# Performance work log

Measured on AMD Instinct MI355X. Metric: run time of the kernel, lower is better.

## Reference

```python
import jax, jax.numpy as jnp
import numpy as np

IN_CH = 4096
OUT_CH = 4096
DENSITY = 0.1
BATCH = 8192


def setup_inputs() -> dict:
    key = jax.random.key(0)
    k_mask, k_w, k_b, k_x = jax.random.split(key, 4)
    # Fixed sparsity pattern, as in the torch module's sparse_mask.nonzero()
    mask = jax.random.bernoulli(k_mask, DENSITY, (OUT_CH, IN_CH))
    rows, cols = jnp.nonzero(mask)  # unique (row, col) pairs
    rows = rows.astype(jnp.int32)
    cols = cols.astype(jnp.int32)
    nnz = rows.shape[0]
    # Kaiming-style init per output row (approximate: uniform bound from mean fan-in)
    fan_in = jnp.maximum(jnp.sum(mask, axis=1).astype(jnp.float32), 1.0)  # [OUT_CH]
    gain = np.sqrt(2.0 / (1.0 + 5.0))  # leaky_relu gain with a=sqrt(5)
    std = gain / jnp.sqrt(fan_in)
    w_bound = np.sqrt(3.0) * std  # per-row bound
    u = jax.random.uniform(k_w, (nnz,), minval=-1.0, maxval=1.0)
    sparse_weight = u * w_bound[rows]
    b_bound = 1.0 / jnp.sqrt(fan_in)
    bias = jax.random.uniform(k_b, (OUT_CH,), minval=-1.0, maxval=1.0) * b_bound
    x = jax.random.normal(k_x, (BATCH, IN_CH), dtype=jnp.float32)
    return {
        "x": x,
        "sparse_weight": sparse_weight.astype(jnp.float32),
        "rows": rows,
        "cols": cols,
        "bias": bias.astype(jnp.float32),
    }


def reference(x, sparse_weight, rows, cols, bias):
    # Rebuild the (fixed-pattern) sparse weight as a dense [OUT_CH, IN_CH] matrix
    # (indices are unique, so .set matches the COO semantics), then y = x @ W^T + b.
    W = jnp.zeros((OUT_CH, IN_CH), dtype=sparse_weight.dtype).at[rows, cols].set(sparse_weight)
    return x @ W.T + bias  # [BATCH, OUT_CH]
```

## Files before the change

### kernel.cpp

```cpp
#include <hip/hip_runtime.h>
#include <hip/hip_bf16.h>

#define M_DIM 8192
#define N_DIM 4096
#define K_DIM 4096
#define BM 128
#define BN 128
#define BK 32

typedef __bf16 bf16x8 __attribute__((ext_vector_type(8)));
typedef float  f32x4  __attribute__((ext_vector_type(4)));
typedef unsigned short u16x8 __attribute__((ext_vector_type(8)));

#define ASYNC16(g, l)                                                          \
  __builtin_amdgcn_global_load_lds(                                            \
      (__attribute__((address_space(1))) void*)(g),                            \
      (__attribute__((address_space(3))) void*)(l), 16, 0, 0)

static __device__ __forceinline__ unsigned short f2bf(float f) {
  unsigned int u = __float_as_uint(f);
  u += 0x7fffu + ((u >> 16) & 1u);
  return (unsigned short)(u >> 16);
}

__global__ __launch_bounds__(256) void sl_prep(
    const float4* __restrict__ x4, u16x8* __restrict__ xb,
    const float* __restrict__ vals, const int* __restrict__ rows,
    const int* __restrict__ cols, unsigned short* __restrict__ W, int nnz) {
  const int b = blockIdx.x;
  if (b < N_DIM) {
    __shared__ __align__(16) unsigned short rowbuf[K_DIM];
    u16x8* rb8 = (u16x8*)rowbuf;
    u16x8 z = {};
    rb8[threadIdx.x] = z;
    rb8[256 + threadIdx.x] = z;
    __syncthreads();
    int l = 0, h = nnz;
    while (l < h) { int m = (l + h) >> 1; if (rows[m] < b) l = m + 1; else h = m; }
    const int s = l;
    h = nnz;
    while (l < h) { int m = (l + h) >> 1; if (rows[m] <= b) l = m + 1; else h = m; }
    const int e = l;
    for (int k = s + threadIdx.x; k < e; k += 256)
      rowbuf[cols[k]] = f2bf(vals[k]);
    __syncthreads();
    u16x8* dst = (u16x8*)(W + (size_t)b * K_DIM);
    dst[threadIdx.x] = rb8[threadIdx.x];
    dst[256 + threadIdx.x] = rb8[256 + threadIdx.x];
  } else {
    const int i = (b - N_DIM) * 256 + threadIdx.x;
    float4 a = x4[2 * i];
    float4 c = x4[2 * i + 1];
    u16x8 o;
    o[0] = f2bf(a.x); o[1] = f2bf(a.y); o[2] = f2bf(a.z); o[3] = f2bf(a.w);
    o[4] = f2bf(c.x); o[5] = f2bf(c.y); o[6] = f2bf(c.z); o[7] = f2bf(c.w);
    xb[i] = o;
  }
}

__global__ __launch_bounds__(256) void sl_gemm_bias(
    const unsigned short* __restrict__ A,
    const unsigned short* __restrict__ B,
    const float* __restrict__ bias,
    float* __restrict__ C) {
  __shared__ __align__(16) unsigned short As[BM * BK];
  __shared__ __align__(16) unsigned short Bs[BN * BK];

  const int tid  = threadIdx.x;
  const int wave = tid >> 6;
  const int lane = tid & 63;
  const int m0 = blockIdx.x * BM;
  const int n0 = blockIdx.y * BN;

  const int srow = tid >> 2;
  const int scol = ((tid & 3) ^ ((tid >> 3) & 3)) * 8;
  const unsigned short* gA0 = A + (size_t)(m0 + srow) * K_DIM + scol;
  const unsigned short* gA1 = gA0 + (size_t)64 * K_DIM;
  const unsigned short* gB0 = B + (size_t)(n0 + srow) * K_DIM + scol;
  const unsigned short* gB1 = gB0 + (size_t)64 * K_DIM;
  unsigned short* lA0 = As + (size_t)(wave * 64) * 8;
  unsigned short* lA1 = As + (size_t)(256 + wave * 64) * 8;
  unsigned short* lB0 = Bs + (size_t)(wave * 64) * 8;
  unsigned short* lB1 = Bs + (size_t)(256 + wave * 64) * 8;

  const int wm   = (wave >> 1) * 64;
  const int wn   = (wave & 1) * 64;
  const int fm   = lane & 15;
  const int quad = lane >> 4;
  const int sw   = (fm >> 1) & 3;
  const int kc   = (quad ^ sw) * 8;

  f32x4 acc[4][4] = {};

  for (int k0 = 0; k0 < K_DIM; k0 += BK) {
    ASYNC16(gA0, lA0);
    ASYNC16(gA1, lA1);
    ASYNC16(gB0, lB0);
    ASYNC16(gB1, lB1);
    gA0 += BK; gA1 += BK; gB0 += BK; gB1 += BK;
    __syncthreads();

    bf16x8 af[4], bfr[4];
#pragma unroll
    for (int t = 0; t < 4; ++t) {
      af[t]  = *(const bf16x8*)(As + (size_t)(wm + t * 16 + fm) * BK + kc);
      bfr[t] = *(const bf16x8*)(Bs + (size_t)(wn + t * 16 + fm) * BK + kc);
    }
#pragma unroll
    for (int tm = 0; tm < 4; ++tm)
#pragma unroll
      for (int tn = 0; tn < 4; ++tn)
        acc[tm][tn] = __builtin_amdgcn_mfma_f32_16x16x32_bf16(
            af[tm], bfr[tn], acc[tm][tn], 0, 0, 0);
    __syncthreads();
  }

  float bv[4];
#pragma unroll
  for (int tn = 0; tn < 4; ++tn) bv[tn] = bias[n0 + wn + tn * 16 + fm];

#pragma unroll
  for (int tm = 0; tm < 4; ++tm) {
    const int mbase = m0 + wm + tm * 16 + quad * 4;
#pragma unroll
    for (int tn = 0; tn < 4; ++tn) {
      const int n = n0 + wn + tn * 16 + fm;
      float* p = C + (size_t)mbase * N_DIM + n;
#pragma unroll
      for (int r = 0; r < 4; ++r)
        p[(size_t)r * N_DIM] = acc[tm][tn][r] + bv[tn];
    }
  }
}

__global__ void sl_naive(const float* __restrict__ x, const float* __restrict__ vals,
                         const int* __restrict__ rows, const int* __restrict__ cols,
                         const float* __restrict__ bias, float* __restrict__ out,
                         int nnz) {
  const int o = blockIdx.x;
  int l = 0, h = nnz;
  while (l < h) { int m = (l + h) >> 1; if (rows[m] < o) l = m + 1; else h = m; }
  const int s = l;
  h = nnz;
  while (l < h) { int m = (l + h) >> 1; if (rows[m] <= o) l = m + 1; else h = m; }
  const int e = l;
  const float bv = bias[o];
  for (int b = threadIdx.x; b < M_DIM; b += blockDim.x) {
    float acc = bv;
    const float* xb = x + (size_t)b * K_DIM;
    for (int k = s; k < e; ++k) acc += vals[k] * xb[cols[k]];
    out[(size_t)b * N_DIM + o] = acc;
  }
}

extern "C" void kernel_launch(void* const* d_in, const int* in_sizes, int n_in,
                              void* d_out, int out_size, void* d_ws, size_t ws_size,
                              hipStream_t stream) {
  const float* x    = (const float*)d_in[0];
  const float* vals = (const float*)d_in[1];
  const int*   rows = (const int*)d_in[2];
  const int*   cols = (const int*)d_in[3];
  const float* bias = (const float*)d_in[4];
  float* out = (float*)d_out;
  const int nnz = in_sizes[1];

  const size_t xb_bytes = (size_t)M_DIM * K_DIM * 2;
  const size_t w_bytes  = (size_t)N_DIM * K_DIM * 2;

  if (ws_size >= xb_bytes + w_bytes) {
    unsigned short* xb = (unsigned short*)d_ws;
    unsigned short* W  = (unsigned short*)((char*)d_ws + xb_bytes);

    const int cvt_blocks = (M_DIM * K_DIM) / 8 / 256;
    sl_prep<<<N_DIM + cvt_blocks, 256, 0, stream>>>(
        (const float4*)x, (u16x8*)xb, vals, rows, cols, W, nnz);
    sl_gemm_bias<<<dim3(M_DIM / BM, N_DIM / BN), 256, 0, stream>>>(xb, W, bias, out);
  } else {
    sl_naive<<<N_DIM, 256, 0, stream>>>(x, vals, rows, cols, bias, out, nnz);
  }
}
```

Before: 561.4 us.

## Double-buffer GEMM K loop with BK=64, precompute row bounds, nontemporal stores

The GEMM tile depth goes from 32 to 64 with a wider XOR swizzle. The loop now issues the next tile's async global-to-LDS loads right after fragments are read into registers, so memory traffic overlaps the MFMA work, and occupancy is hinted at 3 blocks. Row start and end offsets are computed once by a small kernel instead of a binary search per block, and output stores use nontemporal hints. This adds a memset and an extra launch, and raises register and LDS pressure.

```diff
diff --git a/kernel.cpp b/kernel.cpp
--- a/kernel.cpp
+++ b/kernel.cpp
@@ -6,7 +6,7 @@
 #define K_DIM 4096
 #define BM 128
 #define BN 128
-#define BK 32
+#define BK 64
 
 typedef __bf16 bf16x8 __attribute__((ext_vector_type(8)));
 typedef float  f32x4  __attribute__((ext_vector_type(4)));
@@ -23,10 +23,20 @@
   return (unsigned short)(u >> 16);
 }
 
+__global__ void sl_bounds(const int* __restrict__ rows, int* __restrict__ row_start,
+                          int* __restrict__ row_end, int nnz) {
+  int k = blockIdx.x * 256 + threadIdx.x;
+  if (k >= nnz) return;
+  int r = rows[k];
+  if (k == 0 || rows[k - 1] != r) row_start[r] = k;
+  if (k == nnz - 1 || rows[k + 1] != r) row_end[r] = k + 1;
+}
+
 __global__ __launch_bounds__(256) void sl_prep(
     const float4* __restrict__ x4, u16x8* __restrict__ xb,
-    const float* __restrict__ vals, const int* __restrict__ rows,
-    const int* __restrict__ cols, unsigned short* __restrict__ W, int nnz) {
+    const float* __restrict__ vals, const int* __restrict__ cols,
+    const int* __restrict__ row_start, const int* __restrict__ row_end,
+    unsigned short* __restrict__ W) {
   const int b = blockIdx.x;
   if (b < N_DIM) {
     __shared__ __align__(16) unsigned short rowbuf[K_DIM];
@@ -35,12 +45,8 @@
     rb8[threadIdx.x] = z;
     rb8[256 + threadIdx.x] = z;
     __syncthreads();
-    int l = 0, h = nnz;
-    while (l < h) { int m = (l + h) >> 1; if (rows[m] < b) l = m + 1; else h = m; }
-    const int s = l;
-    h = nnz;
-    while (l < h) { int m = (l + h) >> 1; if (rows[m] <= b) l = m + 1; else h = m; }
-    const int e = l;
+    const int s = row_start[b];
+    const int e = row_end[b];
     for (int k = s + threadIdx.x; k < e; k += 256)
       rowbuf[cols[k]] = f2bf(vals[k]);
     __syncthreads();
@@ -58,7 +64,42 @@
   }
 }
 
-__global__ __launch_bounds__(256) void sl_gemm_bias(
+__global__ __launch_bounds__(256) void sl_prep_bs(
+    const float4* __restrict__ x4, u16x8* __restrict__ xb,
+    const float* __restrict__ vals, const int* __restrict__ rows,
+    const int* __restrict__ cols, unsigned short* __restrict__ W, int nnz) {
+  const int b = blockIdx.x;
+  if (b < N_DIM) {
+    __shared__ __align__(16) unsigned short rowbuf[K_DIM];
+    u16x8* rb8 = (u16x8*)rowbuf;
+    u16x8 z = {};
+    rb8[threadIdx.x] = z;
+    rb8[256 + threadIdx.x] = z;
+    __syncthreads();
+    int l = 0, h = nnz;
+    while (l < h) { int m = (l + h) >> 1; if (rows[m] < b) l = m + 1; else h = m; }
+    const int s = l;
+    h = nnz;
+    while (l < h) { int m = (l + h) >> 1; if (rows[m] <= b) l = m + 1; else h = m; }
+    const int e = l;
+    for (int k = s + threadIdx.x; k < e; k += 256)
+      rowbuf[cols[k]] = f2bf(vals[k]);
+    __syncthreads();
+    u16x8* dst = (u16x8*)(W + (size_t)b * K_DIM);
+    dst[threadIdx.x] = rb8[threadIdx.x];
+    dst[256 + threadIdx.x] = rb8[256 + threadIdx.x];
+  } else {
+    const int i = (b - N_DIM) * 256 + threadIdx.x;
+    float4 a = x4[2 * i];
+    float4 c = x4[2 * i + 1];
+    u16x8 o;
+    o[0] = f2bf(a.x); o[1] = f2bf(a.y); o[2] = f2bf(a.z); o[3] = f2bf(a.w);
+    o[4] = f2bf(c.x); o[5] = f2bf(c.y); o[6] = f2bf(c.z); o[7] = f2bf(c.w);
+    xb[i] = o;
+  }
+}
+
+__global__ __launch_bounds__(256, 3) void sl_gemm_bias(
     const unsigned short* __restrict__ A,
     const unsigned short* __restrict__ B,
     const float* __restrict__ bias,
@@ -72,47 +113,62 @@
   const int m0 = blockIdx.x * BM;
   const int n0 = blockIdx.y * BN;
 
-  const int srow = tid >> 2;
-  const int scol = ((tid & 3) ^ ((tid >> 3) & 3)) * 8;
-  const unsigned short* gA0 = A + (size_t)(m0 + srow) * K_DIM + scol;
-  const unsigned short* gA1 = gA0 + (size_t)64 * K_DIM;
-  const unsigned short* gB0 = B + (size_t)(n0 + srow) * K_DIM + scol;
-  const unsigned short* gB1 = gB0 + (size_t)64 * K_DIM;
-  unsigned short* lA0 = As + (size_t)(wave * 64) * 8;
-  unsigned short* lA1 = As + (size_t)(256 + wave * 64) * 8;
-  unsigned short* lB0 = Bs + (size_t)(wave * 64) * 8;
-  unsigned short* lB1 = Bs + (size_t)(256 + wave * 64) * 8;
+  const int srow = tid >> 3;
+  const int scol = ((tid & 7) ^ ((tid >> 3) & 7)) * 8;
+  const unsigned short* gA = A + (size_t)(m0 + srow) * K_DIM + scol;
+  const unsigned short* gB = B + (size_t)(n0 + srow) * K_DIM + scol;
+  unsigned short* lA = As + (size_t)(wave * 64) * 8;
+  unsigned short* lB = Bs + (size_t)(wave * 64) * 8;
+  const size_t GROW = (size_t)32 * K_DIM;
+  const size_t LROW = (size_t)256 * 8;
 
   const int wm   = (wave >> 1) * 64;
   const int wn   = (wave & 1) * 64;
   const int fm   = lane & 15;
   const int quad = lane >> 4;
-  const int sw   = (fm >> 1) & 3;
-  const int kc   = (quad ^ sw) * 8;
+  const int sw   = fm & 7;
 
   f32x4 acc[4][4] = {};
 
+#pragma unroll
+  for (int r = 0; r < 4; ++r) {
+    ASYNC16(gA + r * GROW, lA + r * LROW);
+    ASYNC16(gB + r * GROW, lB + r * LROW);
+  }
+  gA += BK; gB += BK;
+
   for (int k0 = 0; k0 < K_DIM; k0 += BK) {
-    ASYNC16(gA0, lA0);
-    ASYNC16(gA1, lA1);
-    ASYNC16(gB0, lB0);
-    ASYNC16(gB1, lB1);
-    gA0 += BK; gA1 += BK; gB0 += BK; gB1 += BK;
-    __syncthreads();
-
-    bf16x8 af[4], bfr[4];
+    __syncthreads();
+
+    bf16x8 af[4][2], bfr[4][2];
 #pragma unroll
     for (int t = 0; t < 4; ++t) {
-      af[t]  = *(const bf16x8*)(As + (size_t)(wm + t * 16 + fm) * BK + kc);
-      bfr[t] = *(const bf16x8*)(Bs + (size_t)(wn + t * 16 + fm) * BK + kc);
+#pragma unroll
+      for (int h = 0; h < 2; ++h) {
+        const int pA = ((h * 4 + quad) ^ sw) * 8;
+        af[t][h]  = *(const bf16x8*)(As + (size_t)(wm + t * 16 + fm) * BK + pA);
+        bfr[t][h] = *(const bf16x8*)(Bs + (size_t)(wn + t * 16 + fm) * BK + pA);
+      }
     }
-#pragma unroll
-    for (int tm = 0; tm < 4; ++tm)
-#pragma unroll
-      for (int tn = 0; tn < 4; ++tn)
-        acc[tm][tn] = __builtin_amdgcn_mfma_f32_16x16x32_bf16(
-            af[tm], bfr[tn], acc[tm][tn], 0, 0, 0);
-    __syncthreads();
+    __syncthreads();
+
+    if (k0 + BK < K_DIM) {
+#pragma unroll
+      for (int r = 0; r < 4; ++r) {
+        ASYNC16(gA + r * GROW, lA + r * LROW);
+        ASYNC16(gB + r * GROW, lB + r * LROW);
+      }
+      gA += BK; gB += BK;
+    }
+
+#pragma unroll
+    for (int h = 0; h < 2; ++h)
+#pragma unroll
+      for (int tm = 0; tm < 4; ++tm)
+#pragma unroll
+        for (int tn = 0; tn < 4; ++tn)
+          acc[tm][tn] = __builtin_amdgcn_mfma_f32_16x16x32_bf16(
+              af[tm][h], bfr[tn][h], acc[tm][tn], 0, 0, 0);
   }
 
   float bv[4];
@@ -128,7 +184,7 @@
       float* p = C + (size_t)mbase * N_DIM + n;
 #pragma unroll
       for (int r = 0; r < 4; ++r)
-        p[(size_t)r * N_DIM] = acc[tm][tn][r] + bv[tn];
+        __builtin_nontemporal_store(acc[tm][tn][r] + bv[tn], p + (size_t)r * N_DIM);
     }
   }
 }
@@ -164,15 +220,27 @@
   float* out = (float*)d_out;
   const int nnz = in_sizes[1];
 
-  const size_t xb_bytes = (size_t)M_DIM * K_DIM * 2;
-  const size_t w_bytes  = (size_t)N_DIM * K_DIM * 2;
-
-  if (ws_size >= xb_bytes + w_bytes) {
+  const size_t xb_bytes  = (size_t)M_DIM * K_DIM * 2;
+  const size_t w_bytes   = (size_t)N_DIM * K_DIM * 2;
+  const size_t idx_bytes = (size_t)2 * N_DIM * 4;
+
+  const int cvt_blocks = (M_DIM * K_DIM) / 8 / 256;
+
+  if (ws_size >= xb_bytes + w_bytes + idx_bytes) {
     unsigned short* xb = (unsigned short*)d_ws;
     unsigned short* W  = (unsigned short*)((char*)d_ws + xb_bytes);
-
-    const int cvt_blocks = (M_DIM * K_DIM) / 8 / 256;
+    int* row_start = (int*)((char*)d_ws + xb_bytes + w_bytes);
+    int* row_end   = row_start + N_DIM;
+
+    hipMemsetAsync(row_start, 0, idx_bytes, stream);
+    sl_bounds<<<(nnz + 255) / 256, 256, 0, stream>>>(rows, row_start, row_end, nnz);
     sl_prep<<<N_DIM + cvt_blocks, 256, 0, stream>>>(
+        (const float4*)x, (u16x8*)xb, vals, cols, row_start, row_end, W);
+    sl_gemm_bias<<<dim3(M_DIM / BM, N_DIM / BN), 256, 0, stream>>>(xb, W, bias, out);
+  } else if (ws_size >= xb_bytes + w_bytes) {
+    unsigned short* xb = (unsigned short*)d_ws;
+    unsigned short* W  = (unsigned short*)((char*)d_ws + xb_bytes);
+    sl_prep_bs<<<N_DIM + cvt_blocks, 256, 0, stream>>>(
         (const float4*)x, (u16x8*)xb, vals, rows, cols, W, nnz);
     sl_gemm_bias<<<dim3(M_DIM / BM, N_DIM / BN), 256, 0, stream>>>(xb, W, bias, out);
   } else {
```

Result: faster. 477.8 us (-14.9%).
